# Performance work log

Measured on AMD Instinct MI355X. Metric: run time of the kernel, lower is better.

## Reference

```python
import jax, jax.numpy as jnp
import numpy as np

IN, H = 23, 64


def _lstm_layer(x, W_ih, W_hh, b_ih, b_hh):
    # x: [B,T,in] ; W_ih: [4H,in] ; W_hh: [4H,H] ; gate order (PyTorch): i,f,g,o
    B = x.shape[0]
    # precompute input contribution for all timesteps (one big GEMM)
    xg = jnp.einsum('bti,gi->btg', x, W_ih) + (b_ih + b_hh)  # [B,T,4H]

    def step(carry, xt):
        h, c = carry
        gates = xt + h @ W_hh.T  # [B,4H]
        i, f, g, o = jnp.split(gates, 4, axis=-1)
        c = jax.nn.sigmoid(f) * c + jax.nn.sigmoid(i) * jnp.tanh(g)
        h = jax.nn.sigmoid(o) * jnp.tanh(c)
        return (h, c), h

    h0 = jnp.zeros((B, H), x.dtype)
    _, hs = jax.lax.scan(step, (h0, h0), jnp.swapaxes(xg, 0, 1))
    return jnp.swapaxes(hs, 0, 1)  # [B,T,H]


def setup_inputs() -> dict:
    key = jax.random.key(0)
    ks = jax.random.split(key, 12)
    s = 1.0 / np.sqrt(H)  # PyTorch LSTM init scale
    x = jax.random.normal(ks[0], (2048, 512, IN), dtype=jnp.float32)
    W_ih0 = jax.random.uniform(ks[1], (4 * H, IN), jnp.float32, -s, s)
    W_hh0 = jax.random.uniform(ks[2], (4 * H, H), jnp.float32, -s, s)
    b_ih0 = jax.random.uniform(ks[3], (4 * H,), jnp.float32, -s, s)
    b_hh0 = jax.random.uniform(ks[4], (4 * H,), jnp.float32, -s, s)
    W_ih1 = jax.random.uniform(ks[5], (4 * H, H), jnp.float32, -s, s)
    W_hh1 = jax.random.uniform(ks[6], (4 * H, H), jnp.float32, -s, s)
    b_ih1 = jax.random.uniform(ks[7], (4 * H,), jnp.float32, -s, s)
    b_hh1 = jax.random.uniform(ks[8], (4 * H,), jnp.float32, -s, s)
    fc_w = jax.random.uniform(ks[9], (1, H), jnp.float32, -s, s)
    fc_b = jax.random.uniform(ks[10], (1,), jnp.float32, -s, s)
    return {"x": x, "W_ih0": W_ih0, "W_hh0": W_hh0, "b_ih0": b_ih0, "b_hh0": b_hh0,
            "W_ih1": W_ih1, "W_hh1": W_hh1, "b_ih1": b_ih1, "b_hh1": b_hh1,
            "fc_w": fc_w, "fc_b": fc_b}


def reference(x, W_ih0, W_hh0, b_ih0, b_hh0, W_ih1, W_hh1, b_ih1, b_hh1, fc_w, fc_b):
    h1 = _lstm_layer(x, W_ih0, W_hh0, b_ih0, b_hh0)   # [B,T,H]
    h2 = _lstm_layer(h1, W_ih1, W_hh1, b_ih1, b_hh1)  # [B,T,H]
    last = h2[:, -1, :]                               # [B,H]
    return last @ fc_w.T + fc_b                       # [B,1]
```

## Files before the change

### kernel.cpp

```cpp
#include <hip/hip_runtime.h>

typedef _Float16 half8 __attribute__((ext_vector_type(8)));
typedef float floatx4 __attribute__((ext_vector_type(4)));

#define NSTEPS 512
#define IN_F   23
#define HSTRIDE 72

#define LOG2E      1.4426950408889634f
#define NEG2LOG2E -2.8853900817779268f

#if __has_builtin(__builtin_amdgcn_exp2f)
#define EXP2(x) __builtin_amdgcn_exp2f(x)
#else
#define EXP2(x) exp2f(x)
#endif

__device__ __forceinline__ float fast_rcp(float x) { return __builtin_amdgcn_rcpf(x); }

#define MFMA2(acc, Ah, Bhi, Blo)                                                   \
    acc = __builtin_amdgcn_mfma_f32_16x16x32_f16((Ah), (Bhi), (acc), 0, 0, 0);     \
    acc = __builtin_amdgcn_mfma_f32_16x16x32_f16((Ah), (Blo), (acc), 0, 0, 0);

__global__ __launch_bounds__(512, 1)
void lstm2_fused(const float* __restrict__ x,
                 const float* __restrict__ Wih0, const float* __restrict__ Whh0,
                 const float* __restrict__ bih0, const float* __restrict__ bhh0,
                 const float* __restrict__ Wih1, const float* __restrict__ Whh1,
                 const float* __restrict__ bih1, const float* __restrict__ bhh1,
                 const float* __restrict__ fcw, const float* __restrict__ fcb,
                 float* __restrict__ out)
{
    __shared__ _Float16 hbuf[2][2][16 * HSTRIDE];
    __shared__ float red[4][16];

    const int tid  = threadIdx.x;
    const int w8   = tid >> 6;
    const int grp  = w8 >> 2;
    const int wg   = w8 & 3;
    const int lane = tid & 63;
    const int l15  = lane & 15;
    const int krow = lane >> 4;
    const int b0   = blockIdx.x * 8;

    half8 wi_h[4][2], wi_l[4][2], wh_h[4][2], wh_l[4][2];
    float bias[4];
    {
        const float* WI = grp ? Wih1 : Wih0;
        const float* WH = grp ? Whh1 : Whh0;
        const float* BI = grp ? bih1 : bih0;
        const float* BH = grp ? bhh1 : bhh0;
        const float gs[4] = {LOG2E, LOG2E, 2.f * LOG2E, LOG2E};
        #pragma unroll
        for (int q = 0; q < 4; ++q) {
            const int g = q * 64 + wg * 16 + l15;
            if (!grp) {
                #pragma unroll
                for (int j = 0; j < 8; ++j) {
                    const int k = krow * 8 + j;
                    const float v = ((k < IN_F) ? WI[g * IN_F + k] : 0.f) * gs[q];
                    const _Float16 hi = (_Float16)v;
                    wi_h[q][0][j] = hi;
                    wi_l[q][0][j] = (_Float16)(v - (float)hi);
                    wi_h[q][1][j] = (_Float16)0.f;
                    wi_l[q][1][j] = (_Float16)0.f;
                }
            } else {
                #pragma unroll
                for (int kk = 0; kk < 2; ++kk) {
                    #pragma unroll
                    for (int j = 0; j < 8; ++j) {
                        const int k = kk * 32 + krow * 8 + j;
                        const float v = WI[g * 64 + k] * gs[q];
                        const _Float16 hi = (_Float16)v;
                        wi_h[q][kk][j] = hi;
                        wi_l[q][kk][j] = (_Float16)(v - (float)hi);
                    }
                }
            }
            #pragma unroll
            for (int kk = 0; kk < 2; ++kk) {
                #pragma unroll
                for (int j = 0; j < 8; ++j) {
                    const int k = kk * 32 + krow * 8 + j;
                    const float v = WH[g * 64 + k] * gs[q];
                    const _Float16 hi = (_Float16)v;
                    wh_h[q][kk][j] = hi;
                    wh_l[q][kk][j] = (_Float16)(v - (float)hi);
                }
            }
            bias[q] = (BI[g] + BH[g]) * gs[q];
        }
    }
    const float fcwv = fcw[wg * 16 + l15];

    floatx4 c = {0.f, 0.f, 0.f, 0.f};
    half8 in0h, in1h;
    half8 hr0h, hr1h;
    #pragma unroll
    for (int j = 0; j < 8; ++j) {
        in0h[j] = (_Float16)0.f; in1h[j] = (_Float16)0.f;
        hr0h[j] = (_Float16)0.f; hr1h[j] = (_Float16)0.f;
    }

    const float* xrow = x + (size_t)(b0 + (l15 & 7)) * (NSTEPS * IN_F);
    float xf[8], xfn[8];
    if (!grp) {
        #pragma unroll
        for (int j = 0; j < 8; ++j) {
            const int k = krow * 8 + j;
            xf[j] = (k < IN_F) ? xrow[k] : 0.f;
        }
    }

    float hv[4] = {0.f, 0.f, 0.f, 0.f};

    for (int i = 0; i <= NSTEPS; ++i) {
        const bool act = grp ? (i >= 1) : (i < NSTEPS);
        if (act) {
            if (!grp) {
                #pragma unroll
                for (int j = 0; j < 8; ++j) in0h[j] = (_Float16)xf[j];
                const int tn = (i + 1 < NSTEPS) ? (i + 1) : i;
                #pragma unroll
                for (int j = 0; j < 8; ++j) {
                    const int k = krow * 8 + j;
                    xfn[j] = (k < IN_F) ? xrow[(size_t)tn * IN_F + k] : 0.f;
                }
            }

            floatx4 acc[4];
            #pragma unroll
            for (int q = 0; q < 4; ++q) {
                floatx4 a = {bias[q], bias[q], bias[q], bias[q]};
                MFMA2(a, in0h, wi_h[q][0], wi_l[q][0]);
                if (grp) { MFMA2(a, in1h, wi_h[q][1], wi_l[q][1]); }
                MFMA2(a, hr0h, wh_h[q][0], wh_l[q][0]);
                MFMA2(a, hr1h, wh_h[q][1], wh_l[q][1]);
                acc[q] = a;
            }

            #pragma unroll
            for (int r = 0; r < 4; ++r) {
                const float iv = fast_rcp(1.f + EXP2(-acc[0][r]));
                const float fv = fast_rcp(1.f + EXP2(-acc[1][r]));
                const float gv = 2.f * fast_rcp(1.f + EXP2(-acc[2][r])) - 1.f;
                const float ov = fast_rcp(1.f + EXP2(-acc[3][r]));
                const float cn = fv * c[r] + iv * gv;
                c[r] = cn;
                hv[r] = ov * (2.f * fast_rcp(1.f + EXP2(NEG2LOG2E * cn)) - 1.f);
            }

            const int wb = grp ? ((i - 1) & 1) : (i & 1);
            _Float16* dst = &hbuf[grp][wb][0];
            #pragma unroll
            for (int r = 0; r < 4; ++r) {
                const int idx = (krow * 4 + r) * HSTRIDE + wg * 16 + l15;
                dst[idx] = (_Float16)hv[r];
            }
        }

        __syncthreads();

        if (!grp) {
            if (i < NSTEPS) {
                const _Float16* sh = &hbuf[0][i & 1][0];
                hr0h = *(const half8*)&sh[l15 * HSTRIDE + krow * 8];
                hr1h = *(const half8*)&sh[l15 * HSTRIDE + 32 + krow * 8];
                #pragma unroll
                for (int j = 0; j < 8; ++j) xf[j] = xfn[j];
            }
        } else {
            if (i < NSTEPS) {
                const _Float16* sh = &hbuf[0][i & 1][0];
                in0h = *(const half8*)&sh[l15 * HSTRIDE + krow * 8];
                in1h = *(const half8*)&sh[l15 * HSTRIDE + 32 + krow * 8];
            }
            if (i >= 1) {
                const _Float16* sh = &hbuf[1][(i - 1) & 1][0];
                hr0h = *(const half8*)&sh[l15 * HSTRIDE + krow * 8];
                hr1h = *(const half8*)&sh[l15 * HSTRIDE + 32 + krow * 8];
            }
        }
    }

    if (grp) {
        float p[4];
        #pragma unroll
        for (int r = 0; r < 4; ++r) p[r] = hv[r] * fcwv;
        #pragma unroll
        for (int off = 1; off < 16; off <<= 1) {
            #pragma unroll
            for (int r = 0; r < 4; ++r)
                p[r] += __shfl_xor(p[r], off, 64);
        }
        if (l15 == 0) {
            #pragma unroll
            for (int r = 0; r < 4; ++r)
                red[wg][krow * 4 + r] = p[r];
        }
    }
    __syncthreads();
    if (tid < 8) {
        float v = fcb[0];
        v += red[0][tid] + red[1][tid] + red[2][tid] + red[3][tid];
        out[b0 + tid] = v;
    }
}

extern "C" void kernel_launch(void* const* d_in, const int* in_sizes, int n_in,
                              void* d_out, int out_size, void* d_ws, size_t ws_size,
                              hipStream_t stream) {
    (void)n_in; (void)d_ws; (void)ws_size; (void)out_size;
    const float* xp    = (const float*)d_in[0];
    const float* Wih0  = (const float*)d_in[1];
    const float* Whh0  = (const float*)d_in[2];
    const float* bih0  = (const float*)d_in[3];
    const float* bhh0  = (const float*)d_in[4];
    const float* Wih1  = (const float*)d_in[5];
    const float* Whh1  = (const float*)d_in[6];
    const float* bih1  = (const float*)d_in[7];
    const float* bhh1  = (const float*)d_in[8];
    const float* fcw   = (const float*)d_in[9];
    const float* fcb   = (const float*)d_in[10];
    float* outp        = (float*)d_out;

    const int B = in_sizes[0] / (NSTEPS * IN_F);
    const int nblocks = B / 8;
    hipLaunchKernelGGL(lstm2_fused, dim3(nblocks), dim3(512), 0, stream,
                       xp, Wih0, Whh0, bih0, bhh0, Wih1, Whh1, bih1, bhh1,
                       fcw, fcb, outp);
}
```

Before: 678.9 us.

## Split LSTM step into two barrier phases to interleave layer0 and layer1 MFMA/activation

Restructures the time loop into two half-phases per step separated by barriers. Layer 0 does its MFMAs in the first phase and its activations in the second, while layer 1 does its activations in the first phase and its MFMAs in the second. This staggers matrix and transcendental work across wave groups so they overlap, and raises MFMA priority with s_setprio. It costs an extra __syncthreads per step, one more iteration, and a single shared buffer for layer 1 with zero-initialised shared memory.

```diff
diff --git a/kernel.cpp b/kernel.cpp
--- a/kernel.cpp
+++ b/kernel.cpp
@@ -31,7 +31,8 @@
                  const float* __restrict__ fcw, const float* __restrict__ fcb,
                  float* __restrict__ out)
 {
-    __shared__ _Float16 hbuf[2][2][16 * HSTRIDE];
+    __shared__ _Float16 h0buf[2][16 * HSTRIDE];
+    __shared__ _Float16 h1buf[16 * HSTRIDE];
     __shared__ float red[4][16];
 
     const int tid  = threadIdx.x;
@@ -42,6 +43,12 @@
     const int l15  = lane & 15;
     const int krow = lane >> 4;
     const int b0   = blockIdx.x * 8;
+
+    {
+        _Float16* z = &h0buf[0][0];
+        for (int idx = tid; idx < 3 * 16 * HSTRIDE; idx += 512)
+            z[idx] = (_Float16)0.f;
+    }
 
     half8 wi_h[4][2], wi_l[4][2], wh_h[4][2], wh_l[4][2];
     float bias[4];
@@ -102,6 +109,9 @@
         in0h[j] = (_Float16)0.f; in1h[j] = (_Float16)0.f;
         hr0h[j] = (_Float16)0.f; hr1h[j] = (_Float16)0.f;
     }
+    floatx4 acc[4];
+    #pragma unroll
+    for (int q = 0; q < 4; ++q) acc[q] = (floatx4){0.f, 0.f, 0.f, 0.f};
 
     const float* xrow = x + (size_t)(b0 + (l15 & 7)) * (NSTEPS * IN_F);
     float xf[8], xfn[8];
@@ -115,12 +125,26 @@
 
     float hv[4] = {0.f, 0.f, 0.f, 0.f};
 
-    for (int i = 0; i <= NSTEPS; ++i) {
-        const bool act = grp ? (i >= 1) : (i < NSTEPS);
-        if (act) {
-            if (!grp) {
+    __syncthreads();
+
+    for (int i = 0; i <= NSTEPS + 1; ++i) {
+        if (!grp) {
+            if (i < NSTEPS) {
+                const _Float16* sh = &h0buf[(i + 1) & 1][0];
+                hr0h = *(const half8*)&sh[l15 * HSTRIDE + krow * 8];
+                hr1h = *(const half8*)&sh[l15 * HSTRIDE + 32 + krow * 8];
                 #pragma unroll
                 for (int j = 0; j < 8; ++j) in0h[j] = (_Float16)xf[j];
+                __builtin_amdgcn_s_setprio(1);
+                #pragma unroll
+                for (int q = 0; q < 4; ++q) {
+                    floatx4 a = {bias[q], bias[q], bias[q], bias[q]};
+                    MFMA2(a, in0h, wi_h[q][0], wi_l[q][0]);
+                    MFMA2(a, hr0h, wh_h[q][0], wh_l[q][0]);
+                    MFMA2(a, hr1h, wh_h[q][1], wh_l[q][1]);
+                    acc[q] = a;
+                }
+                __builtin_amdgcn_s_setprio(0);
                 const int tn = (i + 1 < NSTEPS) ? (i + 1) : i;
                 #pragma unroll
                 for (int j = 0; j < 8; ++j) {
@@ -128,35 +152,23 @@
                     xfn[j] = (k < IN_F) ? xrow[(size_t)tn * IN_F + k] : 0.f;
                 }
             }
-
-            floatx4 acc[4];
-            #pragma unroll
-            for (int q = 0; q < 4; ++q) {
-                floatx4 a = {bias[q], bias[q], bias[q], bias[q]};
-                MFMA2(a, in0h, wi_h[q][0], wi_l[q][0]);
-                if (grp) { MFMA2(a, in1h, wi_h[q][1], wi_l[q][1]); }
-                MFMA2(a, hr0h, wh_h[q][0], wh_l[q][0]);
-                MFMA2(a, hr1h, wh_h[q][1], wh_l[q][1]);
-                acc[q] = a;
-            }
-
-            #pragma unroll
-            for (int r = 0; r < 4; ++r) {
-                const float iv = fast_rcp(1.f + EXP2(-acc[0][r]));
-                const float fv = fast_rcp(1.f + EXP2(-acc[1][r]));
-                const float gv = 2.f * fast_rcp(1.f + EXP2(-acc[2][r])) - 1.f;
-                const float ov = fast_rcp(1.f + EXP2(-acc[3][r]));
-                const float cn = fv * c[r] + iv * gv;
-                c[r] = cn;
-                hv[r] = ov * (2.f * fast_rcp(1.f + EXP2(NEG2LOG2E * cn)) - 1.f);
-            }
-
-            const int wb = grp ? ((i - 1) & 1) : (i & 1);
-            _Float16* dst = &hbuf[grp][wb][0];
-            #pragma unroll
-            for (int r = 0; r < 4; ++r) {
-                const int idx = (krow * 4 + r) * HSTRIDE + wg * 16 + l15;
-                dst[idx] = (_Float16)hv[r];
+        } else {
+            if (i >= 2) {
+                #pragma unroll
+                for (int r = 0; r < 4; ++r) {
+                    const float iv = fast_rcp(1.f + EXP2(-acc[0][r]));
+                    const float fv = fast_rcp(1.f + EXP2(-acc[1][r]));
+                    const float gv = 2.f * fast_rcp(1.f + EXP2(-acc[2][r])) - 1.f;
+                    const float ov = fast_rcp(1.f + EXP2(-acc[3][r]));
+                    const float cn = fv * c[r] + iv * gv;
+                    c[r] = cn;
+                    hv[r] = ov * (2.f * fast_rcp(1.f + EXP2(NEG2LOG2E * cn)) - 1.f);
+                }
+                #pragma unroll
+                for (int r = 0; r < 4; ++r) {
+                    const int idx = (krow * 4 + r) * HSTRIDE + wg * 16 + l15;
+                    h1buf[idx] = (_Float16)hv[r];
+                }
             }
         }
 
@@ -164,24 +176,48 @@
 
         if (!grp) {
             if (i < NSTEPS) {
-                const _Float16* sh = &hbuf[0][i & 1][0];
-                hr0h = *(const half8*)&sh[l15 * HSTRIDE + krow * 8];
-                hr1h = *(const half8*)&sh[l15 * HSTRIDE + 32 + krow * 8];
+                float h0v[4];
+                #pragma unroll
+                for (int r = 0; r < 4; ++r) {
+                    const float iv = fast_rcp(1.f + EXP2(-acc[0][r]));
+                    const float fv = fast_rcp(1.f + EXP2(-acc[1][r]));
+                    const float gv = 2.f * fast_rcp(1.f + EXP2(-acc[2][r])) - 1.f;
+                    const float ov = fast_rcp(1.f + EXP2(-acc[3][r]));
+                    const float cn = fv * c[r] + iv * gv;
+                    c[r] = cn;
+                    h0v[r] = ov * (2.f * fast_rcp(1.f + EXP2(NEG2LOG2E * cn)) - 1.f);
+                }
+                _Float16* dst = &h0buf[i & 1][0];
+                #pragma unroll
+                for (int r = 0; r < 4; ++r) {
+                    const int idx = (krow * 4 + r) * HSTRIDE + wg * 16 + l15;
+                    dst[idx] = (_Float16)h0v[r];
+                }
                 #pragma unroll
                 for (int j = 0; j < 8; ++j) xf[j] = xfn[j];
             }
         } else {
-            if (i < NSTEPS) {
-                const _Float16* sh = &hbuf[0][i & 1][0];
-                in0h = *(const half8*)&sh[l15 * HSTRIDE + krow * 8];
-                in1h = *(const half8*)&sh[l15 * HSTRIDE + 32 + krow * 8];
-            }
-            if (i >= 1) {
-                const _Float16* sh = &hbuf[1][(i - 1) & 1][0];
-                hr0h = *(const half8*)&sh[l15 * HSTRIDE + krow * 8];
-                hr1h = *(const half8*)&sh[l15 * HSTRIDE + 32 + krow * 8];
-            }
-        }
+            if (i >= 1 && i <= NSTEPS) {
+                const _Float16* sh0 = &h0buf[(i + 1) & 1][0];
+                in0h = *(const half8*)&sh0[l15 * HSTRIDE + krow * 8];
+                in1h = *(const half8*)&sh0[l15 * HSTRIDE + 32 + krow * 8];
+                hr0h = *(const half8*)&h1buf[l15 * HSTRIDE + krow * 8];
+                hr1h = *(const half8*)&h1buf[l15 * HSTRIDE + 32 + krow * 8];
+                __builtin_amdgcn_s_setprio(1);
+                #pragma unroll
+                for (int q = 0; q < 4; ++q) {
+                    floatx4 a = {bias[q], bias[q], bias[q], bias[q]};
+                    MFMA2(a, in0h, wi_h[q][0], wi_l[q][0]);
+                    MFMA2(a, in1h, wi_h[q][1], wi_l[q][1]);
+                    MFMA2(a, hr0h, wh_h[q][0], wh_l[q][0]);
+                    MFMA2(a, hr1h, wh_h[q][1], wh_l[q][1]);
+                    acc[q] = a;
+                }
+                __builtin_amdgcn_s_setprio(0);
+            }
+        }
+
+        __syncthreads();
     }
 
     if (grp) {
```

New measurement: 695.9 us. +2.5%, slower.
